# Kernel tuning notes

Measured on AMD Instinct MI355X. Metric: run time of the kernel, lower is better.

Reference implementation:

```python
import jax, jax.numpy as jnp
import numpy as np

H = 1024   # hidden_size
I = 512    # intermediate_size
E = 16     # num_routed_experts
K = 4      # top-k
B, S = 2, 1024


def setup_inputs() -> dict:
    key = jax.random.key(0)
    ks = jax.random.split(key, 8)
    scale = 0.05  # keep gate logits in a sane range for sigmoid
    return {
        "hidden_states": jax.random.normal(ks[0], (B, S, H), dtype=jnp.float32),
        "gate_w": jax.random.normal(ks[1], (E, H), dtype=jnp.float32) * scale,
        "Wg": jax.random.normal(ks[2], (E, H, I), dtype=jnp.float32) * scale,
        "Wu": jax.random.normal(ks[3], (E, H, I), dtype=jnp.float32) * scale,
        "Wd": jax.random.normal(ks[4], (E, I, H), dtype=jnp.float32) * scale,
        "sg": jax.random.normal(ks[5], (H, I), dtype=jnp.float32) * scale,
        "su": jax.random.normal(ks[6], (H, I), dtype=jnp.float32) * scale,
        "sd": jax.random.normal(ks[7], (I, H), dtype=jnp.float32) * scale,
    }


def reference(hidden_states, gate_w, Wg, Wu, Wd, sg, su, sd):
    b, s, h = hidden_states.shape
    x = hidden_states.reshape(-1, h)                      # [T,H]
    T = x.shape[0]

    # --- routing: top-k sigmoid gating, normalized ---
    scores = jax.nn.sigmoid(x @ gate_w.T)                 # [T,E]
    topk_w, topk_ids = jax.lax.top_k(scores, K)           # [T,K]
    topk_w = topk_w / topk_w.sum(-1, keepdims=True)
    # combine matrix: comb[t,e] = normalized weight if e selected else 0
    comb = jnp.zeros((T, E), dtype=x.dtype).at[jnp.arange(T)[:, None], topk_ids].add(topk_w)

    # --- routed experts: dense per-expert SwiGLU, masked combine ---
    # (mathematically identical to the sorted grouped-GEMM dispatch: tokens
    # not routed to an expert get combine weight 0)
    g = jnp.einsum('th,ehi->tei', x, Wg)                  # [T,E,I]
    u = jnp.einsum('th,ehi->tei', x, Wu)                  # [T,E,I]
    eo = jnp.einsum('tei,eih->teh', jax.nn.silu(g) * u, Wd)  # [T,E,H]
    routed = jnp.einsum('teh,te->th', eo, comb)           # [T,H]

    # --- shared expert SwiGLU ---
    shared = (jax.nn.silu(x @ sg) * (x @ su)) @ sd        # [T,H]

    return (shared + routed).reshape(b, s, h)
```

## Files before the change

### kernel.cpp

```cpp
#include <hip/hip_runtime.h>
#include <math.h>

#define HDIM 1024
#define IDIM 512
#define NEXP 16
#define TOPK 4
#define NTOK 2048
#define NSLOT (NTOK * TOPK)
#define HROWS (NSLOT + NTOK)

typedef __attribute__((ext_vector_type(8))) short s16x8;
typedef __attribute__((ext_vector_type(4))) float f32x4;
typedef __attribute__((ext_vector_type(4))) unsigned short u16x4;

__device__ inline unsigned short bf16_rne(float f) {
    unsigned int u = __float_as_uint(f);
    u += 0x7FFF + ((u >> 16) & 1);
    return (unsigned short)(u >> 16);
}
__device__ inline float bf16_up(unsigned short h) {
    return __uint_as_float(((unsigned int)h) << 16);
}
__device__ inline int swz4(int n) { return (n & 3) ^ ((n >> 2) & 3); }

typedef __attribute__((address_space(3))) unsigned int lds_uint_t;
typedef __attribute__((address_space(1))) unsigned int glob_uint_t;
#define GLD16(gsrc, ldst) __builtin_amdgcn_global_load_lds( \
    (const glob_uint_t*)(gsrc), (lds_uint_t*)(ldst), 16, 0, 0)

#define PLANE_W  ((size_t)17 * 512 * 1024)
#define O_CNT    ((size_t)0)
#define O_TOK    ((size_t)256)
#define O_WGT    (O_TOK + (size_t)17 * NTOK * 4)
#define O_XH     (O_WGT + (size_t)17 * NTOK * 4)
#define O_XL     (O_XH + (size_t)NTOK * HDIM * 2)
#define O_WG_H   (O_XL + (size_t)NTOK * HDIM * 2)
#define O_WG_L   (O_WG_H + PLANE_W * 2)
#define O_WU_H   (O_WG_L + PLANE_W * 2)
#define O_WU_L   (O_WU_H + PLANE_W * 2)
#define O_WD_H   (O_WU_L + PLANE_W * 2)
#define O_WD_L   (O_WD_H + PLANE_W * 2)
#define O_HH     (O_WD_L + PLANE_W * 2)
#define O_HL     (O_HH + (size_t)HROWS * IDIM * 2)
#define FAST_NEED (O_HL + (size_t)HROWS * IDIM * 2)

__global__ __launch_bounds__(64) void route_kernel(const float* __restrict__ x,
                                                   const float* __restrict__ gw,
                                                   int* __restrict__ cnt,
                                                   int* __restrict__ tok,
                                                   float* __restrict__ wgt) {
    const int t = blockIdx.x;
    const int lane = threadIdx.x;
    const float* xr = x + (size_t)t * HDIM;

    float acc[NEXP];
#pragma unroll
    for (int e = 0; e < NEXP; ++e) acc[e] = 0.f;
    for (int h = lane; h < HDIM; h += 64) {
        float xv = xr[h];
#pragma unroll
        for (int e = 0; e < NEXP; ++e) acc[e] += xv * gw[e * HDIM + h];
    }
#pragma unroll
    for (int e = 0; e < NEXP; ++e) {
        float v = acc[e];
#pragma unroll
        for (int off = 32; off > 0; off >>= 1) v += __shfl_xor(v, off, 64);
        acc[e] = v;
    }
    if (lane == 0) {
        float s[NEXP];
#pragma unroll
        for (int e = 0; e < NEXP; ++e) s[e] = 1.f / (1.f + expf(-acc[e]));
        bool used[NEXP];
#pragma unroll
        for (int e = 0; e < NEXP; ++e) used[e] = false;
        int id4[TOPK]; float w4[TOPK]; float sum = 0.f;
        for (int k = 0; k < TOPK; ++k) {
            float best = -1.f; int bi = 0;
            for (int e = 0; e < NEXP; ++e)
                if (!used[e] && s[e] > best) { best = s[e]; bi = e; }
            used[bi] = true; id4[k] = bi; w4[k] = best; sum += best;
        }
        float inv = 1.f / sum;
        for (int k = 0; k < TOPK; ++k) {
            int e = id4[k];
            int slot = atomicAdd(&cnt[e], 1);
            tok[e * NTOK + slot] = (t << 2) | k;
            wgt[e * NTOK + slot] = w4[k] * inv;
        }
    }
}


__global__ __launch_bounds__(256) void conv_act(const float* __restrict__ x,
                                                unsigned short* __restrict__ xh,
                                                unsigned short* __restrict__ xl,
                                                int* __restrict__ cnt,
                                                int* __restrict__ tok,
                                                float* __restrict__ wgt) {
    const int t = blockIdx.x;
    const int tid = threadIdx.x;
    if (tid == 0) {
        tok[16 * NTOK + t] = (t << 2);
        wgt[16 * NTOK + t] = 1.0f;
        if (t == 0) cnt[16] = NTOK;
    }
    const float* src = x + (size_t)t * HDIM;
    unsigned short* dh = xh + (size_t)t * HDIM;
    unsigned short* dl = xl + (size_t)t * HDIM;
    int i = tid * 4;
    f32x4 v = *(const f32x4*)(src + i);
    u16x4 hv, lv;
#pragma unroll
    for (int j = 0; j < 4; ++j) {
        unsigned short h = bf16_rne(v[j]);
        hv[j] = h;
        lv[j] = bf16_rne(v[j] - bf16_up(h));
    }
    *(u16x4*)(dh + i) = hv;
    *(u16x4*)(dl + i) = lv;
}

__global__ __launch_bounds__(256) void conv_w(const float* __restrict__ Wm,
                                              const float* __restrict__ Ws,
                                              unsigned short* __restrict__ dh,
                                              unsigned short* __restrict__ dl,
                                              int K, int N) {
    __shared__ float tile[64][129];
    const int k0 = blockIdx.x * 64, n0 = blockIdx.y * 128, z = blockIdx.z;
    const float* src = (z < 16) ? (Wm + (size_t)z * K * N) : Ws;
    const size_t dbase = (size_t)z * 512 * 1024;
    const int tid = threadIdx.x;

#pragma unroll
    for (int i = 0; i < 8; ++i) {
        int v = tid + i * 256;
        int k = v >> 5, nv = v & 31;
        f32x4 t4 = *(const f32x4*)(src + (size_t)(k0 + k) * N + n0 + nv * 4);
#pragma unroll
        for (int j = 0; j < 4; ++j) tile[k][nv * 4 + j] = t4[j];
    }
    __syncthreads();
#pragma unroll
    for (int i = 0; i < 4; ++i) {
        int c = tid + i * 256;
        int n = c >> 3, dc = c & 7;
        int tl = dc >> 2, kg = dc & 3;
        int ng = n0 + n;
        s16x8 hv, lv;
#pragma unroll
        for (int j = 0; j < 8; ++j) {
            float f = tile[tl * 32 + kg * 8 + j][n];
            unsigned short h = bf16_rne(f);
            hv[j] = (short)h;
            lv[j] = (short)bf16_rne(f - bf16_up(h));
        }
        size_t off = dbase + (size_t)ng * K + k0 + tl * 32 + ((kg ^ swz4(ng)) << 3);
        *(s16x8*)(dh + off) = hv;
        *(s16x8*)(dl + off) = lv;
    }
}

template<bool UP>
__global__ __launch_bounds__(256, 2) void moe_gemm(
        const unsigned short* __restrict__ Ah, const unsigned short* __restrict__ Al,
        const unsigned short* __restrict__ B1h, const unsigned short* __restrict__ B1l,
        const unsigned short* __restrict__ B2h, const unsigned short* __restrict__ B2l,
        const int* __restrict__ cnt, const int* __restrict__ tok,
        const float* __restrict__ wgt,
        unsigned short* __restrict__ Hh, unsigned short* __restrict__ Hl,
        float* __restrict__ out) {
    constexpr int KD = UP ? HDIM : IDIM;
    constexpr int NT = KD / 32;
    constexpr int NP = UP ? 4 : 2;

    const int e = blockIdx.x;
    const int nt = cnt[e];
    const int m0 = blockIdx.y * 128;
    if (m0 >= nt) return;
    const int n0 = blockIdx.z * 64;

    __shared__ unsigned short Bb[2][NP][64 * 32];
    __shared__ int pk[128];
    __shared__ float wts[128];

    const int tid = threadIdx.x;
    for (int i = tid; i < 128; i += 256) {
        int s = m0 + i;
        pk[i] = (s < nt) ? tok[e * NTOK + s] : -1;
        wts[i] = (s < nt) ? wgt[e * NTOK + s] : 0.f;
    }
    __syncthreads();

    const int lane = tid & 63, wid = tid >> 6;
    const int wr = wid >> 1, wc = wid & 1;
    const int lr = lane & 15, kg = lane >> 4;

    const unsigned short* pAh[4];
    const unsigned short* pAl[4];
#pragma unroll
    for (int fm = 0; fm < 4; ++fm) {
        int m = wr * 64 + fm * 16 + lr;
        int p = pk[m];
        size_t row;
        if (UP) row = (p >= 0) ? (size_t)(p >> 2) : 0;
        else    row = (p < 0) ? 0 : (size_t)((e == 16) ? (NSLOT + (p >> 2)) : p);
        pAh[fm] = Ah + row * KD;
        pAl[fm] = Al + row * KD;
    }

    const size_t eoff = (size_t)e * 512 * 1024;
    const unsigned short* bp[4];
    bp[0] = B1h + eoff;
    bp[1] = B1l + eoff;
    if (UP) { bp[2] = B2h + eoff; bp[3] = B2l + eoff; }
    const size_t soff = (size_t)(n0 + (tid >> 2)) * KD + ((tid & 3) << 3);

    f32x4 acc1[4][2], acc2[4][2];
#pragma unroll
    for (int i = 0; i < 4; ++i)
#pragma unroll
        for (int j = 0; j < 2; ++j) {
            acc1[i][j] = (f32x4){0.f, 0.f, 0.f, 0.f};
            if (UP) acc2[i][j] = (f32x4){0.f, 0.f, 0.f, 0.f};
        }

#define STAGE(buf, k0)                                            \
    {                                                             \
        _Pragma("unroll")                                         \
        for (int pl = 0; pl < NP; ++pl)                           \
            GLD16(bp[pl] + soff + (k0), &Bb[buf][pl][tid << 3]);  \
    }

#define COMPUTE(buf, k0)                                                          \
    {                                                                             \
        s16x8 ah[4], al[4];                                                       \
        _Pragma("unroll")                                                         \
        for (int fm = 0; fm < 4; ++fm) {                                          \
            ah[fm] = *(const s16x8*)(pAh[fm] + (k0) + (kg << 3));                 \
            al[fm] = *(const s16x8*)(pAl[fm] + (k0) + (kg << 3));                 \
        }                                                                         \
        _Pragma("unroll")                                                         \
        for (int fn = 0; fn < 2; ++fn) {                                          \
            int nl = wc * 32 + fn * 16 + lr;                                      \
            int off = (nl << 5) + ((kg ^ swz4(nl)) << 3);                         \
            s16x8 b1h = *(const s16x8*)&Bb[buf][0][off];                          \
            s16x8 b1l = *(const s16x8*)&Bb[buf][1][off];                          \
            _Pragma("unroll")                                                     \
            for (int fm = 0; fm < 4; ++fm) {                                      \
                acc1[fm][fn] = __builtin_amdgcn_mfma_f32_16x16x32_bf16(           \
                    ah[fm], b1h, acc1[fm][fn], 0, 0, 0);                          \
                acc1[fm][fn] = __builtin_amdgcn_mfma_f32_16x16x32_bf16(           \
                    ah[fm], b1l, acc1[fm][fn], 0, 0, 0);                          \
                acc1[fm][fn] = __builtin_amdgcn_mfma_f32_16x16x32_bf16(           \
                    al[fm], b1h, acc1[fm][fn], 0, 0, 0);                          \
            }                                                                     \
            if (UP) {                                                             \
                s16x8 b2h = *(const s16x8*)&Bb[buf][NP - 2][off];                 \
                s16x8 b2l = *(const s16x8*)&Bb[buf][NP - 1][off];                 \
                _Pragma("unroll")                                                 \
                for (int fm = 0; fm < 4; ++fm) {                                  \
                    acc2[fm][fn] = __builtin_amdgcn_mfma_f32_16x16x32_bf16(       \
                        ah[fm], b2h, acc2[fm][fn], 0, 0, 0);                      \
                    acc2[fm][fn] = __builtin_amdgcn_mfma_f32_16x16x32_bf16(       \
                        ah[fm], b2l, acc2[fm][fn], 0, 0, 0);                      \
                    acc2[fm][fn] = __builtin_amdgcn_mfma_f32_16x16x32_bf16(       \
                        al[fm], b2h, acc2[fm][fn], 0, 0, 0);                      \
                }                                                                 \
            }                                                                     \
        }                                                                         \
    }

    STAGE(0, 0);
    __syncthreads();
    int cur = 0;
    for (int t = 0; t < NT - 1; ++t) {
        STAGE(cur ^ 1, (t + 1) * 32);
        COMPUTE(cur, t * 32);
        __syncthreads();
        cur ^= 1;
    }
    COMPUTE(cur, (NT - 1) * 32);

#undef STAGE
#undef COMPUTE

#pragma unroll
    for (int fm = 0; fm < 4; ++fm) {
#pragma unroll
        for (int r = 0; r < 4; ++r) {
            int m = wr * 64 + fm * 16 + kg * 4 + r;
            int p = pk[m];
            if (p < 0) continue;
            if (UP) {
                size_t hrow = (e == 16) ? (size_t)(NSLOT + (p >> 2)) : (size_t)p;
#pragma unroll
                for (int fn = 0; fn < 2; ++fn) {
                    int col = n0 + wc * 32 + fn * 16 + lr;
                    float g = acc1[fm][fn][r], u = acc2[fm][fn][r];
                    float v = (g / (1.f + expf(-g))) * u;
                    unsigned short h = bf16_rne(v);
                    Hh[hrow * IDIM + col] = h;
                    Hl[hrow * IDIM + col] = bf16_rne(v - bf16_up(h));
                }
            } else {
                int tkn = p >> 2;
                float w = wts[m];
#pragma unroll
                for (int fn = 0; fn < 2; ++fn) {
                    int col = n0 + wc * 32 + fn * 16 + lr;
                    atomicAdd(&out[(size_t)tkn * HDIM + col], w * acc1[fm][fn][r]);
                }
            }
        }
    }
}

#define FB_CNT_OFF   0
#define FB_TOK_OFF   256
#define FB_WGT_OFF   (FB_TOK_OFF + NEXP * NTOK * 4)
#define FB_HS_OFF    (FB_WGT_OFF + NEXP * NTOK * 4)
#define FB_HR_OFF    (FB_HS_OFF + NTOK * IDIM * 4)

template<bool ROUTED>
__global__ __launch_bounds__(256) void fb_up(const float* __restrict__ A,
                                             const float* __restrict__ W1,
                                             const float* __restrict__ W2,
                                             const int* __restrict__ cnt,
                                             const int* __restrict__ tok,
                                             float* __restrict__ Hout) {
    int e = 0, nt = NTOK, m0, n0;
    if (ROUTED) {
        e = blockIdx.x; nt = cnt[e]; m0 = blockIdx.y * 128;
        if (m0 >= nt) return;
        n0 = blockIdx.z * 128;
    } else { m0 = blockIdx.x * 128; n0 = blockIdx.y * 128; }

    __shared__ unsigned short Ahi[128 * 32], Alo[128 * 32];
    __shared__ unsigned short B1hi[128 * 32], B1lo[128 * 32];
    __shared__ unsigned short B2hi[128 * 32], B2lo[128 * 32];
    __shared__ int pk[128];
    const int tid = threadIdx.x;
    if (ROUTED) {
        for (int i = tid; i < 128; i += 256) {
            int s = m0 + i;
            pk[i] = (s < nt) ? tok[e * NTOK + s] : -1;
        }
        __syncthreads();
    }
    const int am = tid >> 1;
    const int akh = (tid & 1) << 4;
    int arow;
    if (ROUTED) { int p = pk[am]; arow = (p >= 0) ? (p >> 2) : -1; }
    else arow = m0 + am;
    const float* aptr = (arow >= 0) ? (A + (size_t)arow * HDIM + akh) : (const float*)0;
    const int bn = tid & 127;
    const int bc0 = tid >> 7;
    const size_t eoffB = ROUTED ? (size_t)e * HDIM * IDIM : 0;
    const float* w1base = W1 + eoffB + n0 + bn;
    const float* w2base = W2 + eoffB + n0 + bn;
    const int lane = tid & 63, wid = tid >> 6;
    const int wr = wid >> 1, wc = wid & 1;
    const int lr = lane & 15, kg = lane >> 4;
    f32x4 accg[4][4], accu[4][4];
#pragma unroll
    for (int i = 0; i < 4; ++i)
#pragma unroll
        for (int j = 0; j < 4; ++j) {
            accg[i][j] = (f32x4){0.f, 0.f, 0.f, 0.f};
            accu[i][j] = (f32x4){0.f, 0.f, 0.f, 0.f};
        }
    for (int k0 = 0; k0 < HDIM; k0 += 32) {
        {
            float v[16];
            if (arow >= 0) {
                const f32x4* p = (const f32x4*)(aptr + k0);
#pragma unroll
                for (int q = 0; q < 4; ++q) { f32x4 t4 = p[q];
#pragma unroll
                    for (int j = 0; j < 4; ++j) v[q * 4 + j] = t4[j]; }
            } else {
#pragma unroll
                for (int q = 0; q < 16; ++q) v[q] = 0.f;
            }
#pragma unroll
            for (int c = 0; c < 2; ++c) {
                s16x8 hi, lo;
#pragma unroll
                for (int j = 0; j < 8; ++j) {
                    float f = v[c * 8 + j];
                    unsigned short h = bf16_rne(f);
                    hi[j] = (short)h;
                    lo[j] = (short)bf16_rne(f - bf16_up(h));
                }
                int cc = (akh >> 3) + c;
                int off = am * 32 + ((cc ^ (am & 3)) << 3);
                *(s16x8*)&Ahi[off] = hi;
                *(s16x8*)&Alo[off] = lo;
            }
        }
#pragma unroll
        for (int p = 0; p < 2; ++p) {
            int c = p * 2 + bc0;
            const float* r1 = w1base + (size_t)(k0 + c * 8) * IDIM;
            const float* r2 = w2base + (size_t)(k0 + c * 8) * IDIM;
            s16x8 h1, l1, h2, l2;
#pragma unroll
            for (int j = 0; j < 8; ++j) {
                float f1 = r1[j * IDIM];
                unsigned short a1 = bf16_rne(f1);
                h1[j] = (short)a1;
                l1[j] = (short)bf16_rne(f1 - bf16_up(a1));
                float f2 = r2[j * IDIM];
                unsigned short a2 = bf16_rne(f2);
                h2[j] = (short)a2;
                l2[j] = (short)bf16_rne(f2 - bf16_up(a2));
            }
            int off = bn * 32 + ((c ^ (bn & 3)) << 3);
            *(s16x8*)&B1hi[off] = h1;
            *(s16x8*)&B1lo[off] = l1;
            *(s16x8*)&B2hi[off] = h2;
            *(s16x8*)&B2lo[off] = l2;
        }
        __syncthreads();
        s16x8 ah[4], al[4];
#pragma unroll
        for (int fm = 0; fm < 4; ++fm) {
            int r = wr * 64 + fm * 16 + lr;
            int off = r * 32 + ((kg ^ (r & 3)) << 3);
            ah[fm] = *(const s16x8*)&Ahi[off];
            al[fm] = *(const s16x8*)&Alo[off];
        }
#pragma unroll
        for (int fn = 0; fn < 4; ++fn) {
            int cix = wc * 64 + fn * 16 + lr;
            int off = cix * 32 + ((kg ^ (cix & 3)) << 3);
            s16x8 b1h = *(const s16x8*)&B1hi[off];
            s16x8 b1l = *(const s16x8*)&B1lo[off];
            s16x8 b2h = *(const s16x8*)&B2hi[off];
            s16x8 b2l = *(const s16x8*)&B2lo[off];
#pragma unroll
            for (int fm = 0; fm < 4; ++fm) {
                accg[fm][fn] = __builtin_amdgcn_mfma_f32_16x16x32_bf16(ah[fm], b1h, accg[fm][fn], 0, 0, 0);
                accg[fm][fn] = __builtin_amdgcn_mfma_f32_16x16x32_bf16(ah[fm], b1l, accg[fm][fn], 0, 0, 0);
                accg[fm][fn] = __builtin_amdgcn_mfma_f32_16x16x32_bf16(al[fm], b1h, accg[fm][fn], 0, 0, 0);
                accu[fm][fn] = __builtin_amdgcn_mfma_f32_16x16x32_bf16(ah[fm], b2h, accu[fm][fn], 0, 0, 0);
                accu[fm][fn] = __builtin_amdgcn_mfma_f32_16x16x32_bf16(ah[fm], b2l, accu[fm][fn], 0, 0, 0);
                accu[fm][fn] = __builtin_amdgcn_mfma_f32_16x16x32_bf16(al[fm], b2h, accu[fm][fn], 0, 0, 0);
            }
        }
        __syncthreads();
    }
#pragma unroll
    for (int fm = 0; fm < 4; ++fm) {
        int mbase = wr * 64 + fm * 16 + kg * 4;
#pragma unroll
        for (int r = 0; r < 4; ++r) {
            int m = mbase + r;
            int orow;
            if (ROUTED) { int p = pk[m]; if (p < 0) continue; orow = p; }
            else orow = m0 + m;
#pragma unroll
            for (int fn = 0; fn < 4; ++fn) {
                float g = accg[fm][fn][r], u = accu[fm][fn][r];
                float sil = g / (1.f + expf(-g));
                Hout[(size_t)orow * IDIM + n0 + wc * 64 + fn * 16 + lr] = sil * u;
            }
        }
    }
}

template<bool ROUTED>
__global__ __launch_bounds__(256) void fb_down(const float* __restrict__ Hin,
                                               const float* __restrict__ Wdn,
                                               const int* __restrict__ cnt,
                                               const int* __restrict__ tok,
                                               const float* __restrict__ wgt,
                                               float* __restrict__ out) {
    int e = 0, nt = NTOK, m0, n0;
    if (ROUTED) {
        e = blockIdx.x; nt = cnt[e]; m0 = blockIdx.y * 128;
        if (m0 >= nt) return;
        n0 = blockIdx.z * 128;
    } else { m0 = blockIdx.x * 128; n0 = blockIdx.y * 128; }

    __shared__ unsigned short Ahi[128 * 32], Alo[128 * 32];
    __shared__ unsigned short Bhi[128 * 32], Blo[128 * 32];
    __shared__ int pk[128];
    __shared__ float wts[128];
    const int tid = threadIdx.x;
    if (ROUTED) {
        for (int i = tid; i < 128; i += 256) {
            int s = m0 + i;
            pk[i] = (s < nt) ? tok[e * NTOK + s] : -1;
            wts[i] = (s < nt) ? wgt[e * NTOK + s] : 0.f;
        }
        __syncthreads();
    }
    const int am = tid >> 1;
    const int akh = (tid & 1) << 4;
    int arow;
    if (ROUTED) arow = pk[am];
    else arow = m0 + am;
    const float* aptr = (arow >= 0) ? (Hin + (size_t)arow * IDIM + akh) : (const float*)0;
    const int bn = tid & 127;
    const int bc0 = tid >> 7;
    const size_t eoffB = ROUTED ? (size_t)e * IDIM * HDIM : 0;
    const float* wbase = Wdn + eoffB + n0 + bn;
    const int lane = tid & 63, wid = tid >> 6;
    const int wr = wid >> 1, wc = wid & 1;
    const int lr = lane & 15, kg = lane >> 4;
    f32x4 acc[4][4];
#pragma unroll
    for (int i = 0; i < 4; ++i)
#pragma unroll
        for (int j = 0; j < 4; ++j) acc[i][j] = (f32x4){0.f, 0.f, 0.f, 0.f};
    for (int k0 = 0; k0 < IDIM; k0 += 32) {
        {
            float v[16];
            if (arow >= 0) {
                const f32x4* p = (const f32x4*)(aptr + k0);
#pragma unroll
                for (int q = 0; q < 4; ++q) { f32x4 t4 = p[q];
#pragma unroll
                    for (int j = 0; j < 4; ++j) v[q * 4 + j] = t4[j]; }
            } else {
#pragma unroll
                for (int q = 0; q < 16; ++q) v[q] = 0.f;
            }
#pragma unroll
            for (int c = 0; c < 2; ++c) {
                s16x8 hi, lo;
#pragma unroll
                for (int j = 0; j < 8; ++j) {
                    float f = v[c * 8 + j];
                    unsigned short h = bf16_rne(f);
                    hi[j] = (short)h;
                    lo[j] = (short)bf16_rne(f - bf16_up(h));
                }
                int cc = (akh >> 3) + c;
                int off = am * 32 + ((cc ^ (am & 3)) << 3);
                *(s16x8*)&Ahi[off] = hi;
                *(s16x8*)&Alo[off] = lo;
            }
        }
#pragma unroll
        for (int p = 0; p < 2; ++p) {
            int c = p * 2 + bc0;
            const float* r1 = wbase + (size_t)(k0 + c * 8) * HDIM;
            s16x8 h1, l1;
#pragma unroll
            for (int j = 0; j < 8; ++j) {
                float f1 = r1[j * HDIM];
                unsigned short a1 = bf16_rne(f1);
                h1[j] = (short)a1;
                l1[j] = (short)bf16_rne(f1 - bf16_up(a1));
            }
            int off = bn * 32 + ((c ^ (bn & 3)) << 3);
            *(s16x8*)&Bhi[off] = h1;
            *(s16x8*)&Blo[off] = l1;
        }
        __syncthreads();
        s16x8 ah[4], al[4];
#pragma unroll
        for (int fm = 0; fm < 4; ++fm) {
            int r = wr * 64 + fm * 16 + lr;
            int off = r * 32 + ((kg ^ (r & 3)) << 3);
            ah[fm] = *(const s16x8*)&Ahi[off];
            al[fm] = *(const s16x8*)&Alo[off];
        }
#pragma unroll
        for (int fn = 0; fn < 4; ++fn) {
            int cix = wc * 64 + fn * 16 + lr;
            int off = cix * 32 + ((kg ^ (cix & 3)) << 3);
            s16x8 bh = *(const s16x8*)&Bhi[off];
            s16x8 bl = *(const s16x8*)&Blo[off];
#pragma unroll
            for (int fm = 0; fm < 4; ++fm) {
                acc[fm][fn] = __builtin_amdgcn_mfma_f32_16x16x32_bf16(ah[fm], bh, acc[fm][fn], 0, 0, 0);
                acc[fm][fn] = __builtin_amdgcn_mfma_f32_16x16x32_bf16(ah[fm], bl, acc[fm][fn], 0, 0, 0);
                acc[fm][fn] = __builtin_amdgcn_mfma_f32_16x16x32_bf16(al[fm], bh, acc[fm][fn], 0, 0, 0);
            }
        }
        __syncthreads();
    }
#pragma unroll
    for (int fm = 0; fm < 4; ++fm) {
        int mbase = wr * 64 + fm * 16 + kg * 4;
#pragma unroll
        for (int r = 0; r < 4; ++r) {
            int m = mbase + r;
#pragma unroll
            for (int fn = 0; fn < 4; ++fn) {
                int col = n0 + wc * 64 + fn * 16 + lr;
                if (ROUTED) {
                    int p = pk[m];
                    if (p < 0) continue;
                    atomicAdd(&out[(size_t)(p >> 2) * HDIM + col], wts[m] * acc[fm][fn][r]);
                } else {
                    out[(size_t)(m0 + m) * HDIM + col] = acc[fm][fn][r];
                }
            }
        }
    }
}

extern "C" void kernel_launch(void* const* d_in, const int* in_sizes, int n_in,
                              void* d_out, int out_size, void* d_ws, size_t ws_size,
                              hipStream_t stream) {
    const float* x  = (const float*)d_in[0];
    const float* gw = (const float*)d_in[1];
    const float* Wg = (const float*)d_in[2];
    const float* Wu = (const float*)d_in[3];
    const float* Wd = (const float*)d_in[4];
    const float* sg = (const float*)d_in[5];
    const float* su = (const float*)d_in[6];
    const float* sd = (const float*)d_in[7];
    float* out = (float*)d_out;
    char* ws = (char*)d_ws;

    if (ws_size >= FAST_NEED) {
        int* cnt   = (int*)(ws + O_CNT);
        int* tok   = (int*)(ws + O_TOK);
        float* wgt = (float*)(ws + O_WGT);
        unsigned short* xh  = (unsigned short*)(ws + O_XH);
        unsigned short* xl  = (unsigned short*)(ws + O_XL);
        unsigned short* wgh = (unsigned short*)(ws + O_WG_H);
        unsigned short* wgl = (unsigned short*)(ws + O_WG_L);
        unsigned short* wuh = (unsigned short*)(ws + O_WU_H);
        unsigned short* wul = (unsigned short*)(ws + O_WU_L);
        unsigned short* wdh = (unsigned short*)(ws + O_WD_H);
        unsigned short* wdl = (unsigned short*)(ws + O_WD_L);
        unsigned short* hh  = (unsigned short*)(ws + O_HH);
        unsigned short* hl  = (unsigned short*)(ws + O_HL);

        hipMemsetAsync(cnt, 0, 128, stream);
        hipMemsetAsync(out, 0, (size_t)out_size * sizeof(float), stream);
        route_kernel<<<NTOK, 64, 0, stream>>>(x, gw, cnt, tok, wgt);
        conv_act<<<NTOK, 256, 0, stream>>>(x, xh, xl, cnt, tok, wgt);
        conv_w<<<dim3(16, 4, 17), 256, 0, stream>>>(Wg, sg, wgh, wgl, 1024, 512);
        conv_w<<<dim3(16, 4, 17), 256, 0, stream>>>(Wu, su, wuh, wul, 1024, 512);
        conv_w<<<dim3(8, 8, 17), 256, 0, stream>>>(Wd, sd, wdh, wdl, 512, 1024);
        moe_gemm<true><<<dim3(17, 16, 8), 256, 0, stream>>>(
            xh, xl, wgh, wgl, wuh, wul, cnt, tok, wgt, hh, hl, nullptr);
        moe_gemm<false><<<dim3(17, 16, 16), 256, 0, stream>>>(
            hh, hl, wdh, wdl, nullptr, nullptr, cnt, tok, wgt, nullptr, nullptr, out);
    } else {
        int* cnt   = (int*)(ws + FB_CNT_OFF);
        int* tok   = (int*)(ws + FB_TOK_OFF);
        float* wgt = (float*)(ws + FB_WGT_OFF);
        float* hs  = (float*)(ws + FB_HS_OFF);
        float* hr  = (float*)(ws + FB_HR_OFF);

        hipMemsetAsync(cnt, 0, NEXP * sizeof(int), stream);
        route_kernel<<<NTOK, 64, 0, stream>>>(x, gw, cnt, tok, wgt);
        fb_up<false><<<dim3(NTOK / 128, IDIM / 128), 256, 0, stream>>>(x, sg, su, cnt, tok, hs);
        fb_down<false><<<dim3(NTOK / 128, HDIM / 128), 256, 0, stream>>>(hs, sd, cnt, tok, wgt, out);
        fb_up<true><<<dim3(NEXP, NTOK / 128, IDIM / 128), 256, 0, stream>>>(x, Wg, Wu, cnt, tok, hr);
        fb_down<true><<<dim3(NEXP, NTOK / 128, HDIM / 128), 256, 0, stream>>>(hr, Wd, cnt, tok, wgt, out);
    }
}
```

Measured before the change: 537.3 us.

## Stage gathered A tiles through LDS and remap grid to XCD-aware 1D schedule

New measurement: 447.3 us. 1.2x faster.

```diff
diff --git a/kernel.cpp b/kernel.cpp
--- a/kernel.cpp
+++ b/kernel.cpp
@@ -175,21 +175,39 @@
     constexpr int NT = KD / 32;
     constexpr int NP = UP ? 4 : 2;
 
-    const int e = blockIdx.x;
+    const int bid = blockIdx.x;
+    const int xcd = bid & 7, s = bid >> 3;
+    int e, m0, n0;
+    if (UP) {
+        if (s < 16) { e = 16; m0 = s * 128; n0 = xcd * 64; }
+        else {
+            int s2 = s - 16;
+            e = (s2 >> 7) * 8 + xcd;
+            int j = s2 & 127;
+            m0 = (j >> 3) * 128; n0 = (j & 7) * 64;
+        }
+    } else {
+        if (s < 32) { e = 16; m0 = (s >> 1) * 128; n0 = ((s & 1) * 8 + xcd) * 64; }
+        else {
+            int s2 = s - 32;
+            e = (s2 >> 8) * 8 + xcd;
+            int j = s2 & 255;
+            m0 = (j >> 4) * 128; n0 = (j & 15) * 64;
+        }
+    }
     const int nt = cnt[e];
-    const int m0 = blockIdx.y * 128;
     if (m0 >= nt) return;
-    const int n0 = blockIdx.z * 64;
-
+
+    __shared__ unsigned short Ab[2][2][128 * 32];
     __shared__ unsigned short Bb[2][NP][64 * 32];
     __shared__ int pk[128];
     __shared__ float wts[128];
 
     const int tid = threadIdx.x;
     for (int i = tid; i < 128; i += 256) {
-        int s = m0 + i;
-        pk[i] = (s < nt) ? tok[e * NTOK + s] : -1;
-        wts[i] = (s < nt) ? wgt[e * NTOK + s] : 0.f;
+        int ss = m0 + i;
+        pk[i] = (ss < nt) ? tok[e * NTOK + ss] : -1;
+        wts[i] = (ss < nt) ? wgt[e * NTOK + ss] : 0.f;
     }
     __syncthreads();
 
@@ -197,17 +215,20 @@
     const int wr = wid >> 1, wc = wid & 1;
     const int lr = lane & 15, kg = lane >> 4;
 
-    const unsigned short* pAh[4];
-    const unsigned short* pAl[4];
-#pragma unroll
-    for (int fm = 0; fm < 4; ++fm) {
-        int m = wr * 64 + fm * 16 + lr;
-        int p = pk[m];
+    const int r0 = tid >> 2;
+    const int kgl = tid & 3;
+    const unsigned short* sA[2][2];
+    int skoff[2];
+#pragma unroll
+    for (int i = 0; i < 2; ++i) {
+        int r = r0 + i * 64;
+        int p = pk[r];
         size_t row;
         if (UP) row = (p >= 0) ? (size_t)(p >> 2) : 0;
         else    row = (p < 0) ? 0 : (size_t)((e == 16) ? (NSLOT + (p >> 2)) : p);
-        pAh[fm] = Ah + row * KD;
-        pAl[fm] = Al + row * KD;
+        sA[i][0] = Ah + row * KD;
+        sA[i][1] = Al + row * KD;
+        skoff[i] = (kgl ^ swz4(r)) << 3;
     }
 
     const size_t eoff = (size_t)e * 512 * 1024;
@@ -226,20 +247,27 @@
             if (UP) acc2[i][j] = (f32x4){0.f, 0.f, 0.f, 0.f};
         }
 
-#define STAGE(buf, k0)                                            \
-    {                                                             \
-        _Pragma("unroll")                                         \
-        for (int pl = 0; pl < NP; ++pl)                           \
-            GLD16(bp[pl] + soff + (k0), &Bb[buf][pl][tid << 3]);  \
-    }
-
-#define COMPUTE(buf, k0)                                                          \
+#define STAGE(buf, k0)                                                        \
+    {                                                                         \
+        _Pragma("unroll")                                                     \
+        for (int i = 0; i < 2; ++i) {                                         \
+            GLD16(sA[i][0] + (k0) + skoff[i], &Ab[buf][0][(tid + i * 256) << 3]); \
+            GLD16(sA[i][1] + (k0) + skoff[i], &Ab[buf][1][(tid + i * 256) << 3]); \
+        }                                                                     \
+        _Pragma("unroll")                                                     \
+        for (int pl = 0; pl < NP; ++pl)                                       \
+            GLD16(bp[pl] + soff + (k0), &Bb[buf][pl][tid << 3]);              \
+    }
+
+#define COMPUTE(buf)                                                              \
     {                                                                             \
         s16x8 ah[4], al[4];                                                       \
         _Pragma("unroll")                                                         \
         for (int fm = 0; fm < 4; ++fm) {                                          \
-            ah[fm] = *(const s16x8*)(pAh[fm] + (k0) + (kg << 3));                 \
-            al[fm] = *(const s16x8*)(pAl[fm] + (k0) + (kg << 3));                 \
+            int m = wr * 64 + fm * 16 + lr;                                       \
+            int aoff = (m << 5) + ((kg ^ swz4(m)) << 3);                          \
+            ah[fm] = *(const s16x8*)&Ab[buf][0][aoff];                            \
+            al[fm] = *(const s16x8*)&Ab[buf][1][aoff];                            \
         }                                                                         \
         _Pragma("unroll")                                                         \
         for (int fn = 0; fn < 2; ++fn) {                                          \
@@ -277,11 +305,11 @@
     int cur = 0;
     for (int t = 0; t < NT - 1; ++t) {
         STAGE(cur ^ 1, (t + 1) * 32);
-        COMPUTE(cur, t * 32);
+        COMPUTE(cur);
         __syncthreads();
         cur ^= 1;
     }
-    COMPUTE(cur, (NT - 1) * 32);
+    COMPUTE(cur);
 
 #undef STAGE
 #undef COMPUTE
@@ -642,9 +670,9 @@
         conv_w<<<dim3(16, 4, 17), 256, 0, stream>>>(Wg, sg, wgh, wgl, 1024, 512);
         conv_w<<<dim3(16, 4, 17), 256, 0, stream>>>(Wu, su, wuh, wul, 1024, 512);
         conv_w<<<dim3(8, 8, 17), 256, 0, stream>>>(Wd, sd, wdh, wdl, 512, 1024);
-        moe_gemm<true><<<dim3(17, 16, 8), 256, 0, stream>>>(
+        moe_gemm<true><<<2176, 256, 0, stream>>>(
             xh, xl, wgh, wgl, wuh, wul, cnt, tok, wgt, hh, hl, nullptr);
-        moe_gemm<false><<<dim3(17, 16, 16), 256, 0, stream>>>(
+        moe_gemm<false><<<4352, 256, 0, stream>>>(
             hh, hl, wdh, wdl, nullptr, nullptr, cnt, tok, wgt, nullptr, nullptr, out);
     } else {
         int* cnt   = (int*)(ws + FB_CNT_OFF);
```
